# Kernel tuning notes

Hardware: AMD Instinct MI355X
Metric: run time of the kernel (lower is better)

The kernel has to match this reference:

```python
import jax, jax.numpy as jnp
import numpy as np

N_NODES = 50000
IN_CH = 128
HID = 128
OUT_CH = 40
N_LAYERS = 3
N_EDGES = 600000


def setup_inputs() -> dict:
    key = jax.random.key(0)
    ks = jax.random.split(key, 4 + 5 * N_LAYERS)
    x = jax.random.normal(ks[0], (N_NODES, IN_CH), dtype=jnp.float32)
    edge_attr = jax.random.normal(ks[1], (N_EDGES, 4), dtype=jnp.float32)
    edge_index = jax.random.randint(ks[2], (2, N_EDGES), 0, N_NODES, dtype=jnp.int64)
    # Per-layer MLP params ([in->hid->hid]); in==hid so stack as [L, d, d].
    def glorot(k, fan_in, fan_out):
        s = jnp.sqrt(2.0 / (fan_in + fan_out)).astype(jnp.float32)
        return jax.random.normal(k, (fan_in, fan_out), dtype=jnp.float32) * s
    W1 = jnp.stack([glorot(ks[3 + i], IN_CH if i == 0 else HID, HID) for i in range(N_LAYERS)])
    b1 = jnp.zeros((N_LAYERS, HID), dtype=jnp.float32)
    W2 = jnp.stack([glorot(ks[3 + N_LAYERS + i], HID, HID) for i in range(N_LAYERS)])
    b2 = jnp.zeros((N_LAYERS, HID), dtype=jnp.float32)
    Wc = glorot(ks[3 + 2 * N_LAYERS], HID, OUT_CH)
    bc = jnp.zeros((OUT_CH,), dtype=jnp.float32)
    return {"x": x, "edge_attr": edge_attr, "edge_index": edge_index,
            "W1": W1, "b1": b1, "W2": W2, "b2": b2, "Wc": Wc, "bc": bc}


def reference(x, edge_attr, edge_index, W1, b1, W2, b2, Wc, bc):
    # GIN node classifier, eval mode (dropout = identity, BN = identity).
    src, dst = edge_index[0], edge_index[1]
    h = x
    for i in range(N_LAYERS):
        # GINConv (eps=0): aggregate sum of neighbor features via scatter-add.
        msgs = h[src]                                   # [E, d] gather
        aggr = jax.ops.segment_sum(msgs, dst, num_segments=N_NODES)  # [N, d]
        z = h + aggr                                    # (1+eps)*x + sum
        z = jax.nn.relu(z @ W1[i] + b1[i])              # MLP hidden
        z = z @ W2[i] + b2[i]                           # MLP out
        h = jax.nn.relu(z)                              # F.relu(conv(...))
    return h @ Wc + bc                                  # [N, OUT_CH]
```

## Files before the change

kernel.cpp:

```cpp
#include <hip/hip_runtime.h>

#define N_NODES 50000
#define IN_CH 128
#define HID 128
#define OUT_CH 40
#define N_LAYERS 3
#define N_EDGES 600000
#define DSTRIDE 64
#define DEGSTRIDE 16
#define NXCD 8
#define CHUNK 6250

typedef __attribute__((ext_vector_type(8))) short short8;
typedef __attribute__((ext_vector_type(4))) float floatx4;

static __device__ __forceinline__ unsigned short f32_to_bf16(float f) {
  unsigned u = __float_as_uint(f);
  unsigned r = 0x7FFFu + ((u >> 16) & 1u);
  return (unsigned short)((u + r) >> 16);
}
static __device__ __forceinline__ float bf16_to_f32(unsigned short h) {
  return __uint_as_float(((unsigned)h) << 16);
}

#define ZERO_BLOCKS 782
__global__ __launch_bounds__(256) void zero_deg_kernel(int* __restrict__ deg) {
  int i = (blockIdx.x * 256 + threadIdx.x) * 4;
  if (i < N_NODES * DEGSTRIDE) *(int4*)(deg + i) = make_int4(0, 0, 0, 0);
}

#define CSRB 1024
#define ECHUNKS 586
#define CONV_BLOCKS 6250
#define W_BLOCKS 408

__global__ __launch_bounds__(256) void prep_csr_kernel(
    const float* __restrict__ x, const float* __restrict__ W1,
    const float* __restrict__ W2, const float* __restrict__ Wc,
    const int* __restrict__ ei, unsigned short* __restrict__ xb,
    unsigned short* __restrict__ WT, unsigned short* __restrict__ WcT,
    unsigned short* __restrict__ hb1, int* __restrict__ deg,
    int* __restrict__ col) {
  const int b = blockIdx.x;
  const int t = threadIdx.x;
  if (b < CSRB) {
    const int lo = (b & 7) * CHUNK;
    const int hi = lo + CHUNK;
    for (int c = (b >> 3); c < ECHUNKS; c += (CSRB >> 3)) {
      int base = (c * 256 + t) * 4;
      if (base >= N_EDGES) continue;
      int4 s4 = *(const int4*)(ei + base);
      int4 d4 = *(const int4*)(ei + N_EDGES + base);
      if (d4.x >= lo && d4.x < hi) {
        int p = atomicAdd(&deg[(size_t)d4.x * DEGSTRIDE], 1);
        col[(size_t)d4.x * DSTRIDE + p] = s4.x;
      }
      if (d4.y >= lo && d4.y < hi) {
        int p = atomicAdd(&deg[(size_t)d4.y * DEGSTRIDE], 1);
        col[(size_t)d4.y * DSTRIDE + p] = s4.y;
      }
      if (d4.z >= lo && d4.z < hi) {
        int p = atomicAdd(&deg[(size_t)d4.z * DEGSTRIDE], 1);
        col[(size_t)d4.z * DSTRIDE + p] = s4.z;
      }
      if (d4.w >= lo && d4.w < hi) {
        int p = atomicAdd(&deg[(size_t)d4.w * DEGSTRIDE], 1);
        col[(size_t)d4.w * DSTRIDE + p] = s4.w;
      }
    }
  } else if (b < CSRB + CONV_BLOCKS) {
    int i = ((b - CSRB) * 256 + t) * 4;
    if (i < N_NODES * 128) {
      float4 v = *(const float4*)(x + i);
      ushort4 o;
      o.x = f32_to_bf16(v.x); o.y = f32_to_bf16(v.y);
      o.z = f32_to_bf16(v.z); o.w = f32_to_bf16(v.w);
      *(ushort4*)(xb + i) = o;
    }
  } else if (b < CSRB + CONV_BLOCKS + W_BLOCKS) {
    int o = (b - CSRB - CONV_BLOCKS) * 256 + t;
    if (o < 6 * 16384) {
      int mat = o >> 14;
      int r = o & 16383;
      int n = r >> 7;
      int k = r & 127;
      const float* W = (mat < 3) ? (W1 + (size_t)mat * 16384)
                                 : (W2 + (size_t)(mat - 3) * 16384);
      WT[(size_t)mat * 16384 + (size_t)n * 128 + k] =
          f32_to_bf16(W[(size_t)k * 128 + n]);
    } else if (o < 6 * 16384 + 48 * 128) {
      int r = o - 6 * 16384;
      int n = r >> 7;
      int k = r & 127;
      float v = (n < OUT_CH) ? Wc[(size_t)k * OUT_CH + n] : 0.0f;
      WcT[(size_t)n * 128 + k] = f32_to_bf16(v);
    }
  } else {
    if (t < 128) xb[(size_t)N_NODES * 128 + t] = 0;
    else hb1[(size_t)N_NODES * 128 + (t - 128)] = 0;
  }
}

#define AGGR_GRID 6256
__global__ __launch_bounds__(256) void aggregate_kernel(
    const unsigned short* __restrict__ h, const int* __restrict__ deg,
    const int* __restrict__ col, unsigned short* __restrict__ z) {
  const int xcd = blockIdx.x & 7;
  const int idx = blockIdx.x >> 3;
  int local = idx * 8 + (threadIdx.x >> 6) * 2;
  if (local >= CHUNK) return;
  int n0 = __builtin_amdgcn_readfirstlane(xcd * CHUNK + local);
  int n1 = n0 + 1;
  int q = threadIdx.x & 63;
  const size_t co = (size_t)q * 2;
  ushort2 sv0 = *(const ushort2*)(h + (size_t)n0 * 128 + co);
  ushort2 sv1 = *(const ushort2*)(h + (size_t)n1 * 128 + co);
  float ax0[4], ay0[4], ax1[4], ay1[4];
#pragma unroll
  for (int k = 0; k < 4; ++k) { ax0[k] = 0.f; ay0[k] = 0.f; ax1[k] = 0.f; ay1[k] = 0.f; }
  ax0[0] = bf16_to_f32(sv0.x);
  ay0[0] = bf16_to_f32(sv0.y);
  ax1[0] = bf16_to_f32(sv1.x);
  ay1[0] = bf16_to_f32(sv1.y);
  int dg0 = __builtin_amdgcn_readfirstlane(deg[(size_t)n0 * DEGSTRIDE]);
  int dg1 = __builtin_amdgcn_readfirstlane(deg[(size_t)n1 * DEGSTRIDE]);
  int cnt = ((dg0 > dg1 ? dg0 : dg1) + 15) & ~15;
  const int* cp0 = col + (size_t)n0 * DSTRIDE;
  const int* cp1 = col + (size_t)n1 * DSTRIDE;
  for (int i = 0; i < cnt; i += 16) {
    int ss0[16], ss1[16];
#pragma unroll
    for (int k = 0; k < 16; ++k) {
      int sl0 = cp0[i + k];
      int sl1 = cp1[i + k];
      ss0[k] = __builtin_amdgcn_readfirstlane((i + k < dg0) ? sl0 : N_NODES);
      ss1[k] = __builtin_amdgcn_readfirstlane((i + k < dg1) ? sl1 : N_NODES);
    }
    ushort2 v0[16], v1[16];
#pragma unroll
    for (int k = 0; k < 16; ++k) {
      v0[k] = *(const ushort2*)(h + (size_t)ss0[k] * 128 + co);
      v1[k] = *(const ushort2*)(h + (size_t)ss1[k] * 128 + co);
    }
#pragma unroll
    for (int k = 0; k < 16; ++k) {
      ax0[k & 3] += bf16_to_f32(v0[k].x);
      ay0[k & 3] += bf16_to_f32(v0[k].y);
      ax1[k & 3] += bf16_to_f32(v1[k].x);
      ay1[k & 3] += bf16_to_f32(v1[k].y);
    }
  }
  float s0x = (ax0[0] + ax0[1]) + (ax0[2] + ax0[3]);
  float s0y = (ay0[0] + ay0[1]) + (ay0[2] + ay0[3]);
  float s1x = (ax1[0] + ax1[1]) + (ax1[2] + ax1[3]);
  float s1y = (ay1[0] + ay1[1]) + (ay1[2] + ay1[3]);
  ushort2 o0, o1;
  o0.x = f32_to_bf16(s0x);
  o0.y = f32_to_bf16(s0y);
  o1.x = f32_to_bf16(s1x);
  o1.y = f32_to_bf16(s1y);
  *(ushort2*)(z + (size_t)n0 * 128 + co) = o0;
  *(ushort2*)(z + (size_t)n1 * 128 + co) = o1;
}

template <bool LAST>
__global__ __launch_bounds__(256) void layer_pair_kernel(
    const unsigned short* __restrict__ A, const unsigned short* __restrict__ WT1,
    const float* __restrict__ b1, const unsigned short* __restrict__ WT2,
    const float* __restrict__ b2, unsigned short* __restrict__ Z,
    const unsigned short* __restrict__ WcT, const float* __restrict__ bc,
    float* __restrict__ out, int M) {
  __shared__ __align__(16) unsigned short Wl[128][136];
  __shared__ __align__(16) unsigned short T[64][136];
  const int tid = threadIdx.x;
  const int w = tid >> 6;
  const int lane = tid & 63;
  const int qg = lane >> 4;
  const int ln = lane & 15;
  const int row0 = blockIdx.x * 64;
  const int rbase = w * 16;
  const int r0 = row0 + rbase + ln;
  const short8 zero8 = {0, 0, 0, 0, 0, 0, 0, 0};

#pragma unroll
  for (int j = 0; j < 8; ++j) {
    int slot = tid + j * 256;
    int row = slot >> 4;
    int kb = slot & 15;
    *(short8*)&Wl[row][kb * 8] = *(const short8*)(WT1 + (size_t)row * 128 + kb * 8);
  }
  __syncthreads();

  floatx4 acc[8];
#pragma unroll
  for (int ct = 0; ct < 8; ++ct) acc[ct] = (floatx4){0.f, 0.f, 0.f, 0.f};
#pragma unroll
  for (int ks = 0; ks < 4; ++ks) {
    const int koff = ks * 32 + qg * 8;
    short8 a = (r0 < M) ? *(const short8*)(A + (size_t)r0 * 128 + koff) : zero8;
#pragma unroll
    for (int ct = 0; ct < 8; ++ct) {
      short8 b = *(const short8*)&Wl[ct * 16 + ln][koff];
      acc[ct] = __builtin_amdgcn_mfma_f32_16x16x32_bf16(a, b, acc[ct], 0, 0, 0);
    }
  }
#pragma unroll
  for (int ct = 0; ct < 8; ++ct) {
    float bv = b1[ct * 16 + ln];
#pragma unroll
    for (int r = 0; r < 4; ++r) {
      float v = fmaxf(acc[ct][r] + bv, 0.0f);
      T[rbase + qg * 4 + r][ct * 16 + ln] = f32_to_bf16(v);
    }
  }

  __syncthreads();
#pragma unroll
  for (int j = 0; j < 8; ++j) {
    int slot = tid + j * 256;
    int row = slot >> 4;
    int kb = slot & 15;
    *(short8*)&Wl[row][kb * 8] = *(const short8*)(WT2 + (size_t)row * 128 + kb * 8);
  }
  __syncthreads();

  floatx4 acc2[8];
#pragma unroll
  for (int ct = 0; ct < 8; ++ct) acc2[ct] = (floatx4){0.f, 0.f, 0.f, 0.f};
#pragma unroll
  for (int ks = 0; ks < 4; ++ks) {
    const int koff = ks * 32 + qg * 8;
    short8 a = *(const short8*)&T[rbase + ln][koff];
#pragma unroll
    for (int ct = 0; ct < 8; ++ct) {
      short8 b = *(const short8*)&Wl[ct * 16 + ln][koff];
      acc2[ct] = __builtin_amdgcn_mfma_f32_16x16x32_bf16(a, b, acc2[ct], 0, 0, 0);
    }
  }
#pragma unroll
  for (int ct = 0; ct < 8; ++ct) {
    float bv = b2[ct * 16 + ln];
#pragma unroll
    for (int r = 0; r < 4; ++r) {
      float v = fmaxf(acc2[ct][r] + bv, 0.0f);
      T[rbase + qg * 4 + r][ct * 16 + ln] = f32_to_bf16(v);
    }
  }

  if (LAST) {
    floatx4 acc3[3];
#pragma unroll
    for (int ct = 0; ct < 3; ++ct) acc3[ct] = (floatx4){0.f, 0.f, 0.f, 0.f};
#pragma unroll
    for (int ks = 0; ks < 4; ++ks) {
      const int koff = ks * 32 + qg * 8;
      short8 a = *(const short8*)&T[rbase + ln][koff];
#pragma unroll
      for (int ct = 0; ct < 3; ++ct) {
        short8 b = *(const short8*)(WcT + (size_t)(ct * 16 + ln) * 128 + koff);
        acc3[ct] = __builtin_amdgcn_mfma_f32_16x16x32_bf16(a, b, acc3[ct], 0, 0, 0);
      }
    }
#pragma unroll
    for (int ct = 0; ct < 3; ++ct) {
      int colg = ct * 16 + ln;
      if (colg < OUT_CH) {
        float bv = bc[colg];
#pragma unroll
        for (int r = 0; r < 4; ++r) {
          int row = row0 + rbase + qg * 4 + r;
          if (row < M) out[(size_t)row * OUT_CH + colg] = acc3[ct][r] + bv;
        }
      }
    }
  } else {
    __syncthreads();
#pragma unroll
    for (int j = 0; j < 4; ++j) {
      int slot = tid + j * 256;
      int row = slot >> 4;
      int kb = slot & 15;
      if (row0 + row < M) {
        short8 v = *(const short8*)&T[row][kb * 8];
        *(short8*)(Z + (size_t)(row0 + row) * 128 + kb * 8) = v;
      }
    }
  }
}

extern "C" void kernel_launch(void* const* d_in, const int* in_sizes, int n_in,
                              void* d_out, int out_size, void* d_ws,
                              size_t ws_size, hipStream_t stream) {
  const float* x = (const float*)d_in[0];
  const int* ei = (const int*)d_in[2];
  const float* W1 = (const float*)d_in[3];
  const float* b1 = (const float*)d_in[4];
  const float* W2 = (const float*)d_in[5];
  const float* b2 = (const float*)d_in[6];
  const float* Wc = (const float*)d_in[7];
  const float* bc = (const float*)d_in[8];
  float* out = (float*)d_out;

  const size_t NF = (size_t)(N_NODES + 1) * 128;
  unsigned short* hb0 = (unsigned short*)d_ws;
  unsigned short* hb1 = hb0 + NF;
  unsigned short* xbf = hb1 + NF;
  unsigned short* WT = xbf + NF;
  unsigned short* WcT = WT + 6 * 16384;
  int* deg = (int*)(WcT + 48 * 128);
  int* col = deg + (size_t)N_NODES * DEGSTRIDE;

  const dim3 blk(256);
  const int pair_grid = (N_NODES + 63) / 64;

  zero_deg_kernel<<<ZERO_BLOCKS, blk, 0, stream>>>(deg);

  prep_csr_kernel<<<CSRB + CONV_BLOCKS + W_BLOCKS + 1, blk, 0, stream>>>(
      x, W1, W2, Wc, ei, xbf, WT, WcT, hb1, deg, col);

  const unsigned short* h = xbf;
  for (int l = 0; l < N_LAYERS; ++l) {
    aggregate_kernel<<<AGGR_GRID, blk, 0, stream>>>(h, deg, col, hb0);
    if (l < N_LAYERS - 1) {
      layer_pair_kernel<false><<<pair_grid, blk, 0, stream>>>(
          hb0, WT + (size_t)l * 16384, b1 + (size_t)l * 128,
          WT + (size_t)(3 + l) * 16384, b2 + (size_t)l * 128, hb1,
          nullptr, nullptr, nullptr, N_NODES);
      h = hb1;
    } else {
      layer_pair_kernel<true><<<pair_grid, blk, 0, stream>>>(
          hb0, WT + (size_t)l * 16384, b1 + (size_t)l * 128,
          WT + (size_t)(3 + l) * 16384, b2 + (size_t)l * 128, nullptr,
          WcT, bc, out, N_NODES);
    }
  }
}
```

Before: 237.2 us.

## Fuse whole GIN pipeline into one persistent cooperative kernel with grid syncs

Replaces the sequence of eight launches (zero, CSR build, three aggregate plus MLP pairs) with a single cooperative persistent kernel. The phases are separated by grid.sync and use grid-stride loops that keep the XCD-aware node partitioning. The goal is to remove per-launch overhead and the tail gaps between kernels. The cost is grid-wide barriers, fewer resident blocks (at most three per CU) to hide gather latency, and the weight matrices being reloaded into LDS for every tile.

```diff
diff --git a/kernel.cpp b/kernel.cpp
--- a/kernel.cpp
+++ b/kernel.cpp
@@ -1,4 +1,7 @@
 #include <hip/hip_runtime.h>
+#include <hip/hip_cooperative_groups.h>
+
+namespace cg = cooperative_groups;
 
 #define N_NODES 50000
 #define IN_CH 128
@@ -8,8 +11,8 @@
 #define N_EDGES 600000
 #define DSTRIDE 64
 #define DEGSTRIDE 16
-#define NXCD 8
 #define CHUNK 6250
+#define W_ITEMS (6 * 16384 + 48 * 128)
 
 typedef __attribute__((ext_vector_type(8))) short short8;
 typedef __attribute__((ext_vector_type(4))) float floatx4;
@@ -23,6 +26,308 @@
   return __uint_as_float(((unsigned)h) << 16);
 }
 
+
+static __device__ __forceinline__ void w_transpose_item(
+    int o, const float* __restrict__ W1, const float* __restrict__ W2,
+    const float* __restrict__ Wc, unsigned short* __restrict__ WT,
+    unsigned short* __restrict__ WcT) {
+  if (o < 6 * 16384) {
+    int mat = o >> 14;
+    int r = o & 16383;
+    int n = r >> 7;
+    int k = r & 127;
+    const float* W = (mat < 3) ? (W1 + (size_t)mat * 16384)
+                               : (W2 + (size_t)(mat - 3) * 16384);
+    WT[(size_t)mat * 16384 + (size_t)n * 128 + k] =
+        f32_to_bf16(W[(size_t)k * 128 + n]);
+  } else if (o < W_ITEMS) {
+    int r = o - 6 * 16384;
+    int n = r >> 7;
+    int k = r & 127;
+    float v = (n < OUT_CH) ? Wc[(size_t)k * OUT_CH + n] : 0.0f;
+    WcT[(size_t)n * 128 + k] = f32_to_bf16(v);
+  }
+}
+
+static __device__ __forceinline__ void csr_quad(
+    int base, int lo, int hi, const int* __restrict__ ei,
+    int* __restrict__ deg, int* __restrict__ col) {
+  int4 s4 = *(const int4*)(ei + base);
+  int4 d4 = *(const int4*)(ei + N_EDGES + base);
+  if (d4.x >= lo && d4.x < hi) {
+    int p = atomicAdd(&deg[(size_t)d4.x * DEGSTRIDE], 1);
+    col[(size_t)d4.x * DSTRIDE + p] = s4.x;
+  }
+  if (d4.y >= lo && d4.y < hi) {
+    int p = atomicAdd(&deg[(size_t)d4.y * DEGSTRIDE], 1);
+    col[(size_t)d4.y * DSTRIDE + p] = s4.y;
+  }
+  if (d4.z >= lo && d4.z < hi) {
+    int p = atomicAdd(&deg[(size_t)d4.z * DEGSTRIDE], 1);
+    col[(size_t)d4.z * DSTRIDE + p] = s4.z;
+  }
+  if (d4.w >= lo && d4.w < hi) {
+    int p = atomicAdd(&deg[(size_t)d4.w * DEGSTRIDE], 1);
+    col[(size_t)d4.w * DSTRIDE + p] = s4.w;
+  }
+}
+
+static __device__ __forceinline__ void aggr2(
+    const unsigned short* __restrict__ h, const int* __restrict__ deg,
+    const int* __restrict__ col, unsigned short* __restrict__ z,
+    int n0raw, int q) {
+  int n0 = __builtin_amdgcn_readfirstlane(n0raw);
+  int n1 = n0 + 1;
+  const size_t co = (size_t)q * 2;
+  ushort2 sv0 = *(const ushort2*)(h + (size_t)n0 * 128 + co);
+  ushort2 sv1 = *(const ushort2*)(h + (size_t)n1 * 128 + co);
+  float ax0[4], ay0[4], ax1[4], ay1[4];
+#pragma unroll
+  for (int k = 0; k < 4; ++k) { ax0[k] = 0.f; ay0[k] = 0.f; ax1[k] = 0.f; ay1[k] = 0.f; }
+  ax0[0] = bf16_to_f32(sv0.x);
+  ay0[0] = bf16_to_f32(sv0.y);
+  ax1[0] = bf16_to_f32(sv1.x);
+  ay1[0] = bf16_to_f32(sv1.y);
+  int dg0 = __builtin_amdgcn_readfirstlane(deg[(size_t)n0 * DEGSTRIDE]);
+  int dg1 = __builtin_amdgcn_readfirstlane(deg[(size_t)n1 * DEGSTRIDE]);
+  int cnt = ((dg0 > dg1 ? dg0 : dg1) + 15) & ~15;
+  const int* cp0 = col + (size_t)n0 * DSTRIDE;
+  const int* cp1 = col + (size_t)n1 * DSTRIDE;
+  for (int i = 0; i < cnt; i += 16) {
+    int ss0[16], ss1[16];
+#pragma unroll
+    for (int k = 0; k < 16; ++k) {
+      int sl0 = cp0[i + k];
+      int sl1 = cp1[i + k];
+      ss0[k] = __builtin_amdgcn_readfirstlane((i + k < dg0) ? sl0 : N_NODES);
+      ss1[k] = __builtin_amdgcn_readfirstlane((i + k < dg1) ? sl1 : N_NODES);
+    }
+    ushort2 v0[16], v1[16];
+#pragma unroll
+    for (int k = 0; k < 16; ++k) {
+      v0[k] = *(const ushort2*)(h + (size_t)ss0[k] * 128 + co);
+      v1[k] = *(const ushort2*)(h + (size_t)ss1[k] * 128 + co);
+    }
+#pragma unroll
+    for (int k = 0; k < 16; ++k) {
+      ax0[k & 3] += bf16_to_f32(v0[k].x);
+      ay0[k & 3] += bf16_to_f32(v0[k].y);
+      ax1[k & 3] += bf16_to_f32(v1[k].x);
+      ay1[k & 3] += bf16_to_f32(v1[k].y);
+    }
+  }
+  ushort2 o0, o1;
+  o0.x = f32_to_bf16((ax0[0] + ax0[1]) + (ax0[2] + ax0[3]));
+  o0.y = f32_to_bf16((ay0[0] + ay0[1]) + (ay0[2] + ay0[3]));
+  o1.x = f32_to_bf16((ax1[0] + ax1[1]) + (ax1[2] + ax1[3]));
+  o1.y = f32_to_bf16((ay1[0] + ay1[1]) + (ay1[2] + ay1[3]));
+  *(ushort2*)(z + (size_t)n0 * 128 + co) = o0;
+  *(ushort2*)(z + (size_t)n1 * 128 + co) = o1;
+}
+
+template <bool LAST>
+static __device__ __forceinline__ void mlp_tile(
+    unsigned short (&Wl)[128][136], unsigned short (&T)[64][136],
+    const unsigned short* __restrict__ A, const unsigned short* __restrict__ WT1,
+    const float* __restrict__ b1, const unsigned short* __restrict__ WT2,
+    const float* __restrict__ b2, unsigned short* __restrict__ Z,
+    const unsigned short* __restrict__ WcT, const float* __restrict__ bc,
+    float* __restrict__ out, int row0, int tid) {
+  const int w = tid >> 6;
+  const int lane = tid & 63;
+  const int qg = lane >> 4;
+  const int ln = lane & 15;
+  const int rbase = w * 16;
+  const int r0 = row0 + rbase + ln;
+  const short8 zero8 = {0, 0, 0, 0, 0, 0, 0, 0};
+
+#pragma unroll
+  for (int j = 0; j < 8; ++j) {
+    int slot = tid + j * 256;
+    int row = slot >> 4;
+    int kb = slot & 15;
+    *(short8*)&Wl[row][kb * 8] = *(const short8*)(WT1 + (size_t)row * 128 + kb * 8);
+  }
+  __syncthreads();
+
+  floatx4 acc[8];
+#pragma unroll
+  for (int ct = 0; ct < 8; ++ct) acc[ct] = (floatx4){0.f, 0.f, 0.f, 0.f};
+#pragma unroll
+  for (int ks = 0; ks < 4; ++ks) {
+    const int koff = ks * 32 + qg * 8;
+    short8 a = (r0 < N_NODES) ? *(const short8*)(A + (size_t)r0 * 128 + koff) : zero8;
+#pragma unroll
+    for (int ct = 0; ct < 8; ++ct) {
+      short8 b = *(const short8*)&Wl[ct * 16 + ln][koff];
+      acc[ct] = __builtin_amdgcn_mfma_f32_16x16x32_bf16(a, b, acc[ct], 0, 0, 0);
+    }
+  }
+#pragma unroll
+  for (int ct = 0; ct < 8; ++ct) {
+    float bv = b1[ct * 16 + ln];
+#pragma unroll
+    for (int r = 0; r < 4; ++r) {
+      float v = fmaxf(acc[ct][r] + bv, 0.0f);
+      T[rbase + qg * 4 + r][ct * 16 + ln] = f32_to_bf16(v);
+    }
+  }
+
+  __syncthreads();
+#pragma unroll
+  for (int j = 0; j < 8; ++j) {
+    int slot = tid + j * 256;
+    int row = slot >> 4;
+    int kb = slot & 15;
+    *(short8*)&Wl[row][kb * 8] = *(const short8*)(WT2 + (size_t)row * 128 + kb * 8);
+  }
+  __syncthreads();
+
+  floatx4 acc2[8];
+#pragma unroll
+  for (int ct = 0; ct < 8; ++ct) acc2[ct] = (floatx4){0.f, 0.f, 0.f, 0.f};
+#pragma unroll
+  for (int ks = 0; ks < 4; ++ks) {
+    const int koff = ks * 32 + qg * 8;
+    short8 a = *(const short8*)&T[rbase + ln][koff];
+#pragma unroll
+    for (int ct = 0; ct < 8; ++ct) {
+      short8 b = *(const short8*)&Wl[ct * 16 + ln][koff];
+      acc2[ct] = __builtin_amdgcn_mfma_f32_16x16x32_bf16(a, b, acc2[ct], 0, 0, 0);
+    }
+  }
+#pragma unroll
+  for (int ct = 0; ct < 8; ++ct) {
+    float bv = b2[ct * 16 + ln];
+#pragma unroll
+    for (int r = 0; r < 4; ++r) {
+      float v = fmaxf(acc2[ct][r] + bv, 0.0f);
+      T[rbase + qg * 4 + r][ct * 16 + ln] = f32_to_bf16(v);
+    }
+  }
+
+  if (LAST) {
+    floatx4 acc3[3];
+#pragma unroll
+    for (int ct = 0; ct < 3; ++ct) acc3[ct] = (floatx4){0.f, 0.f, 0.f, 0.f};
+#pragma unroll
+    for (int ks = 0; ks < 4; ++ks) {
+      const int koff = ks * 32 + qg * 8;
+      short8 a = *(const short8*)&T[rbase + ln][koff];
+#pragma unroll
+      for (int ct = 0; ct < 3; ++ct) {
+        short8 b = *(const short8*)(WcT + (size_t)(ct * 16 + ln) * 128 + koff);
+        acc3[ct] = __builtin_amdgcn_mfma_f32_16x16x32_bf16(a, b, acc3[ct], 0, 0, 0);
+      }
+    }
+#pragma unroll
+    for (int ct = 0; ct < 3; ++ct) {
+      int colg = ct * 16 + ln;
+      if (colg < OUT_CH) {
+        float bv = bc[colg];
+#pragma unroll
+        for (int r = 0; r < 4; ++r) {
+          int row = row0 + rbase + qg * 4 + r;
+          if (row < N_NODES) out[(size_t)row * OUT_CH + colg] = acc3[ct][r] + bv;
+        }
+      }
+    }
+  } else {
+    __syncthreads();
+#pragma unroll
+    for (int j = 0; j < 4; ++j) {
+      int slot = tid + j * 256;
+      int row = slot >> 4;
+      int kb = slot & 15;
+      if (row0 + row < N_NODES) {
+        short8 v = *(const short8*)&T[row][kb * 8];
+        *(short8*)(Z + (size_t)(row0 + row) * 128 + kb * 8) = v;
+      }
+    }
+  }
+}
+
+__global__ __launch_bounds__(256) void gin_coop_kernel(
+    const float* __restrict__ x, const float* __restrict__ W1,
+    const float* __restrict__ W2, const float* __restrict__ Wc,
+    const int* __restrict__ ei, const float* __restrict__ b1f,
+    const float* __restrict__ b2f, const float* __restrict__ bcf,
+    unsigned short* __restrict__ xbf, unsigned short* __restrict__ WT,
+    unsigned short* __restrict__ WcT, unsigned short* __restrict__ hb0,
+    unsigned short* __restrict__ hb1, int* __restrict__ deg,
+    int* __restrict__ col, float* __restrict__ out) {
+  cg::grid_group grid = cg::this_grid();
+  __shared__ __align__(16) unsigned short Wl[128][136];
+  __shared__ __align__(16) unsigned short T[64][136];
+  const int nb = (int)gridDim.x;
+  const int bid = (int)blockIdx.x;
+  const int tid = (int)threadIdx.x;
+  const int nthreads = nb * 256;
+
+  for (int i = (bid * 256 + tid) * 4; i < N_NODES * DEGSTRIDE; i += nthreads * 4)
+    *(int4*)(deg + i) = make_int4(0, 0, 0, 0);
+  if (bid == 0) {
+    if (tid < 128) xbf[(size_t)N_NODES * 128 + tid] = 0;
+    else hb1[(size_t)N_NODES * 128 + (tid - 128)] = 0;
+  }
+  grid.sync();
+
+  const int csrb = nb >> 1;
+  if (bid < csrb) {
+    const int cls = bid & 7;
+    const int lo = cls * CHUNK, hi = lo + CHUNK;
+    const int stride = (csrb >> 3) * 256 * 4;
+    for (int base = (((bid >> 3) * 256) + tid) * 4; base < N_EDGES; base += stride)
+      csr_quad(base, lo, hi, ei, deg, col);
+  } else {
+    const int sb = bid - csrb;
+    const int sthreads = (nb - csrb) * 256;
+    for (int i = (sb * 256 + tid) * 4; i < N_NODES * 128; i += sthreads * 4) {
+      float4 v = *(const float4*)(x + i);
+      ushort4 o;
+      o.x = f32_to_bf16(v.x); o.y = f32_to_bf16(v.y);
+      o.z = f32_to_bf16(v.z); o.w = f32_to_bf16(v.w);
+      *(ushort4*)(xbf + i) = o;
+    }
+    for (int o = sb * 256 + tid; o < W_ITEMS; o += sthreads)
+      w_transpose_item(o, W1, W2, Wc, WT, WcT);
+  }
+  grid.sync();
+
+  const unsigned short* h = xbf;
+  for (int l = 0; l < N_LAYERS; ++l) {
+    {
+      const int xcd = bid & 7;
+      const int wpx = (nb >> 3) * 4;
+      const int wv = (bid >> 3) * 4 + (tid >> 6);
+      const int q = tid & 63;
+      for (int local = wv * 2; local < CHUNK; local += wpx * 2)
+        aggr2(h, deg, col, hb0, xcd * CHUNK + local, q);
+    }
+    grid.sync();
+    const unsigned short* WT1 = WT + (size_t)l * 16384;
+    const unsigned short* WT2 = WT + (size_t)(3 + l) * 16384;
+    const float* b1 = b1f + (size_t)l * 128;
+    const float* b2 = b2f + (size_t)l * 128;
+    const int ntiles = (N_NODES + 63) / 64;
+    if (l < N_LAYERS - 1) {
+      for (int tile = bid; tile < ntiles; tile += nb) {
+        __syncthreads();
+        mlp_tile<false>(Wl, T, hb0, WT1, b1, WT2, b2, hb1, nullptr, nullptr,
+                        nullptr, tile * 64, tid);
+      }
+      grid.sync();
+      h = hb1;
+    } else {
+      for (int tile = bid; tile < ntiles; tile += nb) {
+        __syncthreads();
+        mlp_tile<true>(Wl, T, hb0, WT1, b1, WT2, b2, nullptr, WcT, bcf, out,
+                       tile * 64, tid);
+      }
+    }
+  }
+}
+
 #define ZERO_BLOCKS 782
 __global__ __launch_bounds__(256) void zero_deg_kernel(int* __restrict__ deg) {
   int i = (blockIdx.x * 256 + threadIdx.x) * 4;
@@ -33,7 +338,6 @@
 #define ECHUNKS 586
 #define CONV_BLOCKS 6250
 #define W_BLOCKS 408
-
 __global__ __launch_bounds__(256) void prep_csr_kernel(
     const float* __restrict__ x, const float* __restrict__ W1,
     const float* __restrict__ W2, const float* __restrict__ Wc,
@@ -49,24 +353,7 @@
     for (int c = (b >> 3); c < ECHUNKS; c += (CSRB >> 3)) {
       int base = (c * 256 + t) * 4;
       if (base >= N_EDGES) continue;
-      int4 s4 = *(const int4*)(ei + base);
-      int4 d4 = *(const int4*)(ei + N_EDGES + base);
-      if (d4.x >= lo && d4.x < hi) {
-        int p = atomicAdd(&deg[(size_t)d4.x * DEGSTRIDE], 1);
-        col[(size_t)d4.x * DSTRIDE + p] = s4.x;
-      }
-      if (d4.y >= lo && d4.y < hi) {
-        int p = atomicAdd(&deg[(size_t)d4.y * DEGSTRIDE], 1);
-        col[(size_t)d4.y * DSTRIDE + p] = s4.y;
-      }
-      if (d4.z >= lo && d4.z < hi) {
-        int p = atomicAdd(&deg[(size_t)d4.z * DEGSTRIDE], 1);
-        col[(size_t)d4.z * DSTRIDE + p] = s4.z;
-      }
-      if (d4.w >= lo && d4.w < hi) {
-        int p = atomicAdd(&deg[(size_t)d4.w * DEGSTRIDE], 1);
-        col[(size_t)d4.w * DSTRIDE + p] = s4.w;
-      }
+      csr_quad(base, lo, hi, ei, deg, col);
     }
   } else if (b < CSRB + CONV_BLOCKS) {
     int i = ((b - CSRB) * 256 + t) * 4;
@@ -78,23 +365,7 @@
       *(ushort4*)(xb + i) = o;
     }
   } else if (b < CSRB + CONV_BLOCKS + W_BLOCKS) {
-    int o = (b - CSRB - CONV_BLOCKS) * 256 + t;
-    if (o < 6 * 16384) {
-      int mat = o >> 14;
-      int r = o & 16383;
-      int n = r >> 7;
-      int k = r & 127;
-      const float* W = (mat < 3) ? (W1 + (size_t)mat * 16384)
-                                 : (W2 + (size_t)(mat - 3) * 16384);
-      WT[(size_t)mat * 16384 + (size_t)n * 128 + k] =
-          f32_to_bf16(W[(size_t)k * 128 + n]);
-    } else if (o < 6 * 16384 + 48 * 128) {
-      int r = o - 6 * 16384;
-      int n = r >> 7;
-      int k = r & 127;
-      float v = (n < OUT_CH) ? Wc[(size_t)k * OUT_CH + n] : 0.0f;
-      WcT[(size_t)n * 128 + k] = f32_to_bf16(v);
-    }
+    w_transpose_item((b - CSRB - CONV_BLOCKS) * 256 + t, W1, W2, Wc, WT, WcT);
   } else {
     if (t < 128) xb[(size_t)N_NODES * 128 + t] = 0;
     else hb1[(size_t)N_NODES * 128 + (t - 128)] = 0;
@@ -109,58 +380,7 @@
   const int idx = blockIdx.x >> 3;
   int local = idx * 8 + (threadIdx.x >> 6) * 2;
   if (local >= CHUNK) return;
-  int n0 = __builtin_amdgcn_readfirstlane(xcd * CHUNK + local);
-  int n1 = n0 + 1;
-  int q = threadIdx.x & 63;
-  const size_t co = (size_t)q * 2;
-  ushort2 sv0 = *(const ushort2*)(h + (size_t)n0 * 128 + co);
-  ushort2 sv1 = *(const ushort2*)(h + (size_t)n1 * 128 + co);
-  float ax0[4], ay0[4], ax1[4], ay1[4];
-#pragma unroll
-  for (int k = 0; k < 4; ++k) { ax0[k] = 0.f; ay0[k] = 0.f; ax1[k] = 0.f; ay1[k] = 0.f; }
-  ax0[0] = bf16_to_f32(sv0.x);
-  ay0[0] = bf16_to_f32(sv0.y);
-  ax1[0] = bf16_to_f32(sv1.x);
-  ay1[0] = bf16_to_f32(sv1.y);
-  int dg0 = __builtin_amdgcn_readfirstlane(deg[(size_t)n0 * DEGSTRIDE]);
-  int dg1 = __builtin_amdgcn_readfirstlane(deg[(size_t)n1 * DEGSTRIDE]);
-  int cnt = ((dg0 > dg1 ? dg0 : dg1) + 15) & ~15;
-  const int* cp0 = col + (size_t)n0 * DSTRIDE;
-  const int* cp1 = col + (size_t)n1 * DSTRIDE;
-  for (int i = 0; i < cnt; i += 16) {
-    int ss0[16], ss1[16];
-#pragma unroll
-    for (int k = 0; k < 16; ++k) {
-      int sl0 = cp0[i + k];
-      int sl1 = cp1[i + k];
-      ss0[k] = __builtin_amdgcn_readfirstlane((i + k < dg0) ? sl0 : N_NODES);
-      ss1[k] = __builtin_amdgcn_readfirstlane((i + k < dg1) ? sl1 : N_NODES);
-    }
-    ushort2 v0[16], v1[16];
-#pragma unroll
-    for (int k = 0; k < 16; ++k) {
-      v0[k] = *(const ushort2*)(h + (size_t)ss0[k] * 128 + co);
-      v1[k] = *(const ushort2*)(h + (size_t)ss1[k] * 128 + co);
-    }
-#pragma unroll
-    for (int k = 0; k < 16; ++k) {
-      ax0[k & 3] += bf16_to_f32(v0[k].x);
-      ay0[k & 3] += bf16_to_f32(v0[k].y);
-      ax1[k & 3] += bf16_to_f32(v1[k].x);
-      ay1[k & 3] += bf16_to_f32(v1[k].y);
-    }
-  }
-  float s0x = (ax0[0] + ax0[1]) + (ax0[2] + ax0[3]);
-  float s0y = (ay0[0] + ay0[1]) + (ay0[2] + ay0[3]);
-  float s1x = (ax1[0] + ax1[1]) + (ax1[2] + ax1[3]);
-  float s1y = (ay1[0] + ay1[1]) + (ay1[2] + ay1[3]);
-  ushort2 o0, o1;
-  o0.x = f32_to_bf16(s0x);
-  o0.y = f32_to_bf16(s0y);
-  o1.x = f32_to_bf16(s1x);
-  o1.y = f32_to_bf16(s1y);
-  *(ushort2*)(z + (size_t)n0 * 128 + co) = o0;
-  *(ushort2*)(z + (size_t)n1 * 128 + co) = o1;
+  aggr2(h, deg, col, z, xcd * CHUNK + local, threadIdx.x & 63);
 }
 
 template <bool LAST>
@@ -169,123 +389,11 @@
     const float* __restrict__ b1, const unsigned short* __restrict__ WT2,
     const float* __restrict__ b2, unsigned short* __restrict__ Z,
     const unsigned short* __restrict__ WcT, const float* __restrict__ bc,
-    float* __restrict__ out, int M) {
+    float* __restrict__ out) {
   __shared__ __align__(16) unsigned short Wl[128][136];
   __shared__ __align__(16) unsigned short T[64][136];
-  const int tid = threadIdx.x;
-  const int w = tid >> 6;
-  const int lane = tid & 63;
-  const int qg = lane >> 4;
-  const int ln = lane & 15;
-  const int row0 = blockIdx.x * 64;
-  const int rbase = w * 16;
-  const int r0 = row0 + rbase + ln;
-  const short8 zero8 = {0, 0, 0, 0, 0, 0, 0, 0};
-
-#pragma unroll
-  for (int j = 0; j < 8; ++j) {
-    int slot = tid + j * 256;
-    int row = slot >> 4;
-    int kb = slot & 15;
-    *(short8*)&Wl[row][kb * 8] = *(const short8*)(WT1 + (size_t)row * 128 + kb * 8);
-  }
-  __syncthreads();
-
-  floatx4 acc[8];
-#pragma unroll
-  for (int ct = 0; ct < 8; ++ct) acc[ct] = (floatx4){0.f, 0.f, 0.f, 0.f};
-#pragma unroll
-  for (int ks = 0; ks < 4; ++ks) {
-    const int koff = ks * 32 + qg * 8;
-    short8 a = (r0 < M) ? *(const short8*)(A + (size_t)r0 * 128 + koff) : zero8;
-#pragma unroll
-    for (int ct = 0; ct < 8; ++ct) {
-      short8 b = *(const short8*)&Wl[ct * 16 + ln][koff];
-      acc[ct] = __builtin_amdgcn_mfma_f32_16x16x32_bf16(a, b, acc[ct], 0, 0, 0);
-    }
-  }
-#pragma unroll
-  for (int ct = 0; ct < 8; ++ct) {
-    float bv = b1[ct * 16 + ln];
-#pragma unroll
-    for (int r = 0; r < 4; ++r) {
-      float v = fmaxf(acc[ct][r] + bv, 0.0f);
-      T[rbase + qg * 4 + r][ct * 16 + ln] = f32_to_bf16(v);
-    }
-  }
-
-  __syncthreads();
-#pragma unroll
-  for (int j = 0; j < 8; ++j) {
-    int slot = tid + j * 256;
-    int row = slot >> 4;
-    int kb = slot & 15;
-    *(short8*)&Wl[row][kb * 8] = *(const short8*)(WT2 + (size_t)row * 128 + kb * 8);
-  }
-  __syncthreads();
-
-  floatx4 acc2[8];
-#pragma unroll
-  for (int ct = 0; ct < 8; ++ct) acc2[ct] = (floatx4){0.f, 0.f, 0.f, 0.f};
-#pragma unroll
-  for (int ks = 0; ks < 4; ++ks) {
-    const int koff = ks * 32 + qg * 8;
-    short8 a = *(const short8*)&T[rbase + ln][koff];
-#pragma unroll
-    for (int ct = 0; ct < 8; ++ct) {
-      short8 b = *(const short8*)&Wl[ct * 16 + ln][koff];
-      acc2[ct] = __builtin_amdgcn_mfma_f32_16x16x32_bf16(a, b, acc2[ct], 0, 0, 0);
-    }
-  }
-#pragma unroll
-  for (int ct = 0; ct < 8; ++ct) {
-    float bv = b2[ct * 16 + ln];
-#pragma unroll
-    for (int r = 0; r < 4; ++r) {
-      float v = fmaxf(acc2[ct][r] + bv, 0.0f);
-      T[rbase + qg * 4 + r][ct * 16 + ln] = f32_to_bf16(v);
-    }
-  }
-
-  if (LAST) {
-    floatx4 acc3[3];
-#pragma unroll
-    for (int ct = 0; ct < 3; ++ct) acc3[ct] = (floatx4){0.f, 0.f, 0.f, 0.f};
-#pragma unroll
-    for (int ks = 0; ks < 4; ++ks) {
-      const int koff = ks * 32 + qg * 8;
-      short8 a = *(const short8*)&T[rbase + ln][koff];
-#pragma unroll
-      for (int ct = 0; ct < 3; ++ct) {
-        short8 b = *(const short8*)(WcT + (size_t)(ct * 16 + ln) * 128 + koff);
-        acc3[ct] = __builtin_amdgcn_mfma_f32_16x16x32_bf16(a, b, acc3[ct], 0, 0, 0);
-      }
-    }
-#pragma unroll
-    for (int ct = 0; ct < 3; ++ct) {
-      int colg = ct * 16 + ln;
-      if (colg < OUT_CH) {
-        float bv = bc[colg];
-#pragma unroll
-        for (int r = 0; r < 4; ++r) {
-          int row = row0 + rbase + qg * 4 + r;
-          if (row < M) out[(size_t)row * OUT_CH + colg] = acc3[ct][r] + bv;
-        }
-      }
-    }
-  } else {
-    __syncthreads();
-#pragma unroll
-    for (int j = 0; j < 4; ++j) {
-      int slot = tid + j * 256;
-      int row = slot >> 4;
-      int kb = slot & 15;
-      if (row0 + row < M) {
-        short8 v = *(const short8*)&T[row][kb * 8];
-        *(short8*)(Z + (size_t)(row0 + row) * 128 + kb * 8) = v;
-      }
-    }
-  }
+  mlp_tile<LAST>(Wl, T, A, WT1, b1, WT2, b2, Z, WcT, bc, out,
+                 blockIdx.x * 64, threadIdx.x);
 }
 
 extern "C" void kernel_launch(void* const* d_in, const int* in_sizes, int n_in,
@@ -310,14 +418,42 @@
   int* deg = (int*)(WcT + 48 * 128);
   int* col = deg + (size_t)N_NODES * DEGSTRIDE;
 
+  static int coop_grid = -1;
+  if (coop_grid == -1) {
+    int dev = 0;
+    hipGetDevice(&dev);
+    int coop = 0;
+    hipDeviceGetAttribute(&coop, hipDeviceAttributeCooperativeLaunch, dev);
+    int ncu = 0;
+    hipDeviceGetAttribute(&ncu, hipDeviceAttributeMultiprocessorCount, dev);
+    int maxb = 0;
+    hipError_t e = hipOccupancyMaxActiveBlocksPerMultiprocessor(
+        &maxb, (const void*)gin_coop_kernel, 256, 0);
+    if (coop && e == hipSuccess && maxb > 0 && ncu > 0) {
+      if (maxb > 3) maxb = 3;
+      coop_grid = ncu * maxb;
+      coop_grid -= coop_grid % 32;
+      if (coop_grid < 32) coop_grid = 0;
+    } else {
+      coop_grid = 0;
+    }
+  }
+
+  if (coop_grid > 0) {
+    void* args[] = {(void*)&x,   (void*)&W1,  (void*)&W2,  (void*)&Wc,
+                    (void*)&ei,  (void*)&b1,  (void*)&b2,  (void*)&bc,
+                    (void*)&xbf, (void*)&WT,  (void*)&WcT, (void*)&hb0,
+                    (void*)&hb1, (void*)&deg, (void*)&col, (void*)&out};
+    hipLaunchCooperativeKernel((const void*)gin_coop_kernel, dim3(coop_grid),
+                               dim3(256), args, 0, stream);
+    return;
+  }
+
   const dim3 blk(256);
   const int pair_grid = (N_NODES + 63) / 64;
-
   zero_deg_kernel<<<ZERO_BLOCKS, blk, 0, stream>>>(deg);
-
   prep_csr_kernel<<<CSRB + CONV_BLOCKS + W_BLOCKS + 1, blk, 0, stream>>>(
       x, W1, W2, Wc, ei, xbf, WT, WcT, hb1, deg, col);
-
   const unsigned short* h = xbf;
   for (int l = 0; l < N_LAYERS; ++l) {
     aggregate_kernel<<<AGGR_GRID, blk, 0, stream>>>(h, deg, col, hb0);
@@ -325,13 +461,13 @@
       layer_pair_kernel<false><<<pair_grid, blk, 0, stream>>>(
           hb0, WT + (size_t)l * 16384, b1 + (size_t)l * 128,
           WT + (size_t)(3 + l) * 16384, b2 + (size_t)l * 128, hb1,
-          nullptr, nullptr, nullptr, N_NODES);
+          nullptr, nullptr, nullptr);
       h = hb1;
     } else {
       layer_pair_kernel<true><<<pair_grid, blk, 0, stream>>>(
           hb0, WT + (size_t)l * 16384, b1 + (size_t)l * 128,
           WT + (size_t)(3 + l) * 16384, b2 + (size_t)l * 128, nullptr,
-          WcT, bc, out, N_NODES);
-    }
-  }
-}
+          WcT, bc, out);
+    }
+  }
+}
```

Measured after the change: 580.9 us. 145% more time.
